# Performance work log

Hardware: AMD Instinct MI355X
Metric: run time of the kernel (lower is better)

Reference implementation:

```python
import jax, jax.numpy as jnp
import numpy as np


def setup_inputs() -> dict:
    key = jax.random.key(0)
    k1, k2 = jax.random.split(key)
    B, C, T, H, W = 4, 256, 8, 32, 32
    K = 1024  # num_embeddings
    z = jax.random.normal(k1, (B, C, T, H, W), dtype=jnp.float32)
    # original init: uniform(-1/K, 1/K)
    emb_weight = jax.random.uniform(k2, (K, C), dtype=jnp.float32,
                                    minval=-1.0 / K, maxval=1.0 / K)
    return {"z": z, "emb_weight": emb_weight}


def reference(z, emb_weight):
    B, C, T, H, W = z.shape
    # (B,C,T,H,W) -> (N, C) with N = B*T*H*W
    z_flat = jnp.transpose(z, (0, 2, 3, 4, 1)).reshape(-1, C)
    # squared L2 distances via ||a||^2 + ||b||^2 - 2 a.b  (fused, vectorized;
    # no python batching loop needed)
    d = (jnp.sum(z_flat * z_flat, axis=1, keepdims=True)
         + jnp.sum(emb_weight * emb_weight, axis=1)
         - 2.0 * z_flat @ emb_weight.T)  # (N, K)
    indices = jnp.argmin(d, axis=1)  # (N,)
    z_q = emb_weight[indices]  # (N, C) gather
    z_q = jnp.transpose(z_q.reshape(B, T, H, W, C), (0, 4, 1, 2, 3))
    # straight-through estimator
    z_q = z + jax.lax.stop_gradient(z_q - z)
    return z_q, indices.reshape(B, T, H, W)
```

## Files before the change

kernel.cpp:

```cpp
#include <hip/hip_runtime.h>
#include <hip/hip_bf16.h>


#define DEVI __device__ __forceinline__

typedef __attribute__((ext_vector_type(8))) short bf16x8;
typedef __attribute__((ext_vector_type(4))) float f32x4;

#define C_DIM   256
#define K_CODES 1024
#define S_DIM   8192
#define N_ROWS  32768
#define ZQ_ELEMS 8388608
#define TILE_M  64
#define NCHUNK  32
#define BAND1   1.0e-3f
#define REC_CAP 8192
#define UCAP    832
#define FLT_BIG 3.402823466e+38f

#define WS_EFR  0
#define WS_E2F  524288
#define WS_CNT  528384
#define WS_REC  528448

DEVI unsigned short f2b(float f) {
    unsigned u = __float_as_uint(f);
    u += 0x7FFFu + ((u >> 16) & 1u);
    return (unsigned short)(u >> 16);
}
DEVI unsigned umin2(unsigned a, unsigned b) { return a < b ? a : b; }
DEVI unsigned umax2(unsigned a, unsigned b) { return a > b ? a : b; }
DEVI unsigned long long ullmin2(unsigned long long a, unsigned long long b) {
    return a < b ? a : b;
}
DEVI float ntl(const float* p) { return __builtin_nontemporal_load(p); }
DEVI void nts(float* p, float v) { __builtin_nontemporal_store(v, p); }

DEVI f32x4 MF(bf16x8 a, bf16x8 b, f32x4 c) {
    return __builtin_amdgcn_mfma_f32_16x16x32_bf16(a, b, c, 0, 0, 0);
}
DEVI bf16x8 ldsfrag(const char* L, int row, int coff) {
    const int byte = row * 512 + (coff ^ ((row & 7) << 4));
    return *reinterpret_cast<const bf16x8*>(L + byte);
}

__global__ void vq_prep(const float* __restrict__ E,
                        unsigned short* __restrict__ efrag,
                        float* __restrict__ e2f, int* __restrict__ gcnt) {
    const int k = blockIdx.x;
    const int lane = threadIdx.x;
    if (k == 0 && lane == 0) *gcnt = 0;
    const float4 v = reinterpret_cast<const float4*>(E + (size_t)k * C_DIM)[lane];
    double s = (double)v.x * v.x + (double)v.y * v.y
             + (double)v.z * v.z + (double)v.w * v.w;
    ushort4 h;
    h.x = f2b(v.x); h.y = f2b(v.y); h.z = f2b(v.z); h.w = f2b(v.w);
    const int f = lane >> 1, half = lane & 1;
    const int ks = f >> 2, q = f & 3;
    const int jj = k & 15, wn = (k >> 4) & 1, chunk = k >> 5;
    char* dst = (char*)efrag + (size_t)chunk * 16384 + wn * 8192
              + ks * 1024 + (q * 16 + jj) * 16 + half * 8;
    *reinterpret_cast<ushort4*>(dst) = h;
#pragma unroll
    for (int m = 32; m; m >>= 1) s += __shfl_xor(s, m, 64);
    if (lane == 0) e2f[k] = (float)s;
}

__global__ __launch_bounds__(256, 2) void vq_main(
        const float* __restrict__ z, const float* __restrict__ E,
        const unsigned short* __restrict__ efrag,
        const float* __restrict__ e2f,
        float* __restrict__ out_zq, float* __restrict__ out_idx,
        int* __restrict__ gcnt, int2* __restrict__ grec) {
    __shared__ __align__(16) char smraw[65792];
    __shared__ float e2p[1024];
    __shared__ int   kfinA[64];
    __shared__ int   flagA[64];
    __shared__ float znS[64];
    __shared__ unsigned long long best64[64];
    __shared__ int   units[UCAP];
    __shared__ int   ucnt;

    const int tid = threadIdx.x;
    const int n0 = blockIdx.x * TILE_M;
    const int b  = n0 >> 13;
    const int s0 = n0 & (S_DIM - 1);

    {
        const float4 v = reinterpret_cast<const float4*>(e2f)[tid];
        float4 w; w.x = 1.0f + v.x; w.y = 1.0f + v.y;
        w.z = 1.0f + v.z; w.w = 1.0f + v.w;
        reinterpret_cast<float4*>(e2p)[tid] = w;
    }

    {
        const int s  = tid & 63;
        const int cg = tid >> 6;
        const float* zb = z + (size_t)b * (C_DIM * S_DIM) + s0 + s;
#pragma unroll
        for (int ci = 0; ci < 16; ++ci) {
            const int c = cg * 4 + ci * 16;
            ushort4 h;
            h.x = f2b(ntl(zb + (size_t)(c + 0) * S_DIM));
            h.y = f2b(ntl(zb + (size_t)(c + 1) * S_DIM));
            h.z = f2b(ntl(zb + (size_t)(c + 2) * S_DIM));
            h.w = f2b(ntl(zb + (size_t)(c + 3) * S_DIM));
            const int byte = s * 512 + ((c * 2) ^ ((s & 7) << 4));
            *reinterpret_cast<ushort4*>(smraw + byte) = h;
        }
    }
    __syncthreads();

    const int w    = tid >> 6;
    const int lane = tid & 63;
    const int wm   = w >> 1, wn = w & 1;
    const int q    = lane >> 4, jj = lane & 15;
    const int mycol = wn * 16 + jj;

    bf16x8 Ah0[8], Ah1[8];
    {
        const int r0 = wm * 32 + jj, r1 = r0 + 16;
#pragma unroll
        for (int ks = 0; ks < 8; ++ks) {
            const int coff = ks * 64 + q * 16;
            Ah0[ks] = ldsfrag(smraw, r0, coff);
            Ah1[ks] = ldsfrag(smraw, r1, coff);
        }
    }

    const char* gB = (const char*)efrag + (size_t)wn * 8192 + (size_t)lane * 16;

#define LOADB(BR, N)                                                          \
    { _Pragma("unroll")                                                       \
      for (int ks_ = 0; ks_ < 8; ++ks_)                                       \
          BR[ks_] = *reinterpret_cast<const bf16x8*>(                         \
              gB + (size_t)(N) * 16384 + ks_ * 1024); }

#define RCOMPUTE(BR, A0, A1)                                                  \
    { A0 = (f32x4){0.f, 0.f, 0.f, 0.f}; A1 = A0;                              \
      _Pragma("unroll")                                                       \
      for (int ks_ = 0; ks_ < 8; ++ks_) {                                     \
          A0 = MF(Ah0[ks_], BR[ks_], A0);                                     \
          A1 = MF(Ah1[ks_], BR[ks_], A1);                                     \
      } }

#define UPD(A0, A1, E2V, N)                                                   \
    { _Pragma("unroll")                                                       \
      for (int r = 0; r < 4; ++r) {                                           \
          unsigned t_ = (__float_as_uint(                                     \
              __builtin_fmaf(-2.f, A0[r], E2V)) & 0xFFFFFFE0u) | (unsigned)(N);\
          unsigned lo_ = umin2(K1[r], t_), hi_ = umax2(K1[r], t_);            \
          K1[r] = lo_; K2[r] = umin2(K2[r], hi_);                             \
          t_ = (__float_as_uint(                                              \
              __builtin_fmaf(-2.f, A1[r], E2V)) & 0xFFFFFFE0u) | (unsigned)(N);\
          lo_ = umin2(K1[4 + r], t_); hi_ = umax2(K1[4 + r], t_);             \
          K1[4 + r] = lo_; K2[4 + r] = umin2(K2[4 + r], hi_);                 \
      } }

    unsigned K1[8], K2[8];
#pragma unroll
    for (int i = 0; i < 8; ++i) { K1[i] = 0xFFFFFFFFu; K2[i] = 0xFFFFFFFFu; }

    bf16x8 Bc[8], Bn[8];
    LOADB(Bc, 0)
    LOADB(Bn, 1)
    f32x4 aA0, aA1, aB0, aB1;

#pragma unroll
    for (int p = 0; p < 16; ++p) {
        const int nA = 2 * p, nB = 2 * p + 1;
        RCOMPUTE(Bc, aA0, aA1)
        if (p < 15) LOADB(Bc, nA + 2)
        UPD(aA0, aA1, e2p[nA * 32 + mycol], nA)
        RCOMPUTE(Bn, aB0, aB1)
        if (p < 15) LOADB(Bn, nB + 2)
        UPD(aB0, aB1, e2p[nB * 32 + mycol], nB)
    }

    __syncthreads();
    if (tid == 0) ucnt = 0;
    for (int i = tid; i < UCAP; i += 256) units[i] = -1;
#pragma unroll
    for (int t = 0; t < 2; ++t) {
#pragma unroll
        for (int r = 0; r < 4; ++r) {
            const int sl = t * 4 + r;
            const int row = wm * 32 + t * 16 + q * 4 + r;
            *reinterpret_cast<int2*>(smraw + row * 272 + mycol * 8) =
                make_int2((int)K1[sl], (int)K2[sl]);
        }
    }
    __syncthreads();

    if (tid < 64) {
        const char* dmp = smraw + tid * 272;
        unsigned kmin = 0xFFFFFFFFu; int emin = 0;
#pragma unroll 4
        for (int e = 0; e < 32; ++e) {
            const unsigned k1 = (unsigned)
                reinterpret_cast<const int2*>(dmp + e * 8)->x;
            if (k1 < kmin) { kmin = k1; emin = e; }
        }
        const int kmincode = (int)((kmin & 31u) << 5) | emin;
        const float dminf = __uint_as_float(kmin & 0xFFFFFFE0u);
        const unsigned limk =
            (__float_as_uint(dminf + BAND1) & 0xFFFFFFE0u) | 31u;
        int cnt = 0, nfb = 0, fb0 = 0, fb1 = 0;
#pragma unroll 4
        for (int e = 0; e < 32; ++e) {
            const int2 v = *reinterpret_cast<const int2*>(dmp + e * 8);
            if ((unsigned)v.x <= limk) {
                const int code = (int)(((unsigned)v.x & 31u) << 5) | e;
                cnt += (code != kmincode);
            }
            if ((unsigned)v.y <= limk) {
                if (nfb == 0) fb0 = e; else if (nfb == 1) fb1 = e;
                ++nfb;
            }
        }
        kfinA[tid] = kmincode;
        flagA[tid] = 0;
        if (cnt > 0 || nfb > 0) {
            bool ov = (cnt > 16 || nfb > 2);
            if (!ov) {
                const int need = 1 + cnt + 32 * nfb;
                const int base = atomicAdd(&ucnt, need);
                if (base + need <= UCAP) {
                    flagA[tid] = 1;
                    best64[tid] = 0xFFFFFFFFFFFFFFFFull;
                    int p = base;
                    units[p++] = (tid << 10) | kmincode;
                    for (int e = 0; e < 32; ++e) {
                        const int2 v = *reinterpret_cast<const int2*>(dmp + e * 8);
                        if ((unsigned)v.x <= limk) {
                            const int code = (int)(((unsigned)v.x & 31u) << 5) | e;
                            if (code != kmincode) units[p++] = (tid << 10) | code;
                        }
                    }
                    if (nfb >= 1)
                        for (int c = 0; c < 32; ++c)
                            units[p++] = (tid << 10) | (c << 5) | fb0;
                    if (nfb >= 2)
                        for (int c = 0; c < 32; ++c)
                            units[p++] = (tid << 10) | (c << 5) | fb1;
                } else ov = true;
            }
            if (ov) {
                const int slot = atomicAdd(gcnt, 1);
                if (slot < REC_CAP) grec[slot] = make_int2(n0 + tid, kmincode);
            }
        }
    }
    __syncthreads();

    {
        const int s  = tid & 63;
        const int cg = tid >> 6;
        const float* zb = z + (size_t)b * (C_DIM * S_DIM) + s0 + s;
        float* zr = reinterpret_cast<float*>(smraw) + s * 257;
#pragma unroll
        for (int ci = 0; ci < 16; ++ci) {
            const int c = cg * 4 + ci * 16;
            zr[c + 0] = ntl(zb + (size_t)(c + 0) * S_DIM);
            zr[c + 1] = ntl(zb + (size_t)(c + 1) * S_DIM);
            zr[c + 2] = ntl(zb + (size_t)(c + 2) * S_DIM);
            zr[c + 3] = ntl(zb + (size_t)(c + 3) * S_DIM);
        }
    }
    __syncthreads();

    if (tid < 64 && flagA[tid]) {
        const float* zr = reinterpret_cast<const float*>(smraw) + tid * 257;
        double a0 = 0.0, a1 = 0.0, a2 = 0.0, a3 = 0.0;
#pragma unroll 8
        for (int c = 0; c < 256; c += 4) {
            const double v0 = zr[c], v1 = zr[c+1], v2 = zr[c+2], v3 = zr[c+3];
            a0 = fma(v0, v0, a0); a1 = fma(v1, v1, a1);
            a2 = fma(v2, v2, a2); a3 = fma(v3, v3, a3);
        }
        znS[tid] = (float)((a0 + a1) + (a2 + a3));
    }
    __syncthreads();

    {
        const int nu = (ucnt < UCAP) ? ucnt : UCAP;
        for (int u = tid; u < nu; u += 256) {
            const int enc = units[u];
            if (enc < 0) continue;
            const int row = enc >> 10, k = enc & 1023;
            const float* zr = reinterpret_cast<const float*>(smraw) + row * 257;
            const float* er = E + (size_t)k * C_DIM;
            double a0 = 0.0, a1 = 0.0, a2 = 0.0, a3 = 0.0;
#pragma unroll 8
            for (int c = 0; c < 256; c += 4) {
                a0 = fma((double)zr[c+0], (double)er[c+0], a0);
                a1 = fma((double)zr[c+1], (double)er[c+1], a1);
                a2 = fma((double)zr[c+2], (double)er[c+2], a2);
                a3 = fma((double)zr[c+3], (double)er[c+3], a3);
            }
            const float t32 = (float)((a0 + a1) + (a2 + a3));
            const float d = (znS[row] + e2f[k]) - 2.0f * t32;
            const unsigned long long key =
                ((unsigned long long)__float_as_uint(d) << 32) | (unsigned)k;
            atomicMin(&best64[row], key);
        }
    }
    __syncthreads();

    if (tid < 64) {
        if (flagA[tid])
            kfinA[tid] = (int)(best64[tid] & 0xFFFFFFFFull);
        nts(out_idx + n0 + tid, (float)kfinA[tid]);
    }

#pragma unroll
    for (int h = 0; h < 2; ++h) {
        __syncthreads();
        {
            const int slot = tid & 31;
            const int cg   = tid >> 5;
            const int kk   = kfinA[h * 32 + slot];
            const float4* er = reinterpret_cast<const float4*>(
                E + (size_t)kk * C_DIM + cg * 32);
            float* lb = reinterpret_cast<float*>(smraw) + slot * 257 + cg * 32;
#pragma unroll
            for (int i = 0; i < 8; ++i) {
                const float4 v = er[i];
                lb[4 * i + 0] = v.x; lb[4 * i + 1] = v.y;
                lb[4 * i + 2] = v.z; lb[4 * i + 3] = v.w;
            }
        }
        __syncthreads();
        {
            const int sg = tid & 31;
            const int cg = tid >> 5;
            float* ob = out_zq + (size_t)b * (C_DIM * S_DIM) + s0 + h * 32 + sg;
            const float* lr = reinterpret_cast<const float*>(smraw) + sg * 257;
#pragma unroll
            for (int i = 0; i < 32; ++i) {
                const int c = cg * 32 + i;
                nts(ob + (size_t)c * S_DIM, lr[c]);
            }
        }
    }
}

__global__ __launch_bounds__(256) void vq_fall(
        const float* __restrict__ z, const float* __restrict__ E,
        const float* __restrict__ e2f,
        const int* __restrict__ gcnt, const int2* __restrict__ grec,
        float* __restrict__ out_zq, float* __restrict__ out_idx) {
    __shared__ float zsh[256];
    __shared__ double dpart[4];
    __shared__ unsigned long long wbest[4];

    const int tid = threadIdx.x;
    const int w = tid >> 6, lane = tid & 63;
    int count = gcnt[0]; if (count > REC_CAP) count = REC_CAP;

    for (int ri = blockIdx.x; ri < count; ri += gridDim.x) {
        const int2 rc = grec[ri];
        const int n = rc.x, kmin = rc.y;
        const int b = n >> 13, s = n & (S_DIM - 1);
        __syncthreads();
        const float zc = z[((size_t)(b * C_DIM + tid)) * S_DIM + s];
        zsh[tid] = zc;
        double p = (double)zc * (double)zc;
#pragma unroll
        for (int m = 32; m; m >>= 1) p += __shfl_xor(p, m, 64);
        if (lane == 0) dpart[w] = p;
        __syncthreads();
        const float znf = (float)((dpart[0] + dpart[1]) + (dpart[2] + dpart[3]));

        unsigned long long best = 0xFFFFFFFFFFFFFFFFull;
        for (int j = 0; j < 4; ++j) {
            const int k = j * 256 + tid;
            const float4* er = reinterpret_cast<const float4*>(
                E + (size_t)k * C_DIM);
            double a0 = 0.0, a1 = 0.0, a2 = 0.0, a3 = 0.0;
#pragma unroll 8
            for (int i = 0; i < 64; ++i) {
                const float4 ev = er[i];
                const float4 zl = reinterpret_cast<const float4*>(zsh)[i];
                a0 = fma((double)zl.x, (double)ev.x, a0);
                a1 = fma((double)zl.y, (double)ev.y, a1);
                a2 = fma((double)zl.z, (double)ev.z, a2);
                a3 = fma((double)zl.w, (double)ev.w, a3);
            }
            const float t32 = (float)((a0 + a1) + (a2 + a3));
            const float d = (znf + e2f[k]) - 2.0f * t32;
            best = ullmin2(best,
                ((unsigned long long)__float_as_uint(d) << 32) | (unsigned)k);
        }
#pragma unroll
        for (int m = 32; m; m >>= 1)
            best = ullmin2(best, (unsigned long long)__shfl_xor(
                (long long)best, m, 64));
        if (lane == 0) wbest[w] = best;
        __syncthreads();
        const unsigned long long fin =
            ullmin2(ullmin2(wbest[0], wbest[1]), ullmin2(wbest[2], wbest[3]));
        const int bk = (int)(fin & 0xFFFFFFFFull);
        if (tid == 0) out_idx[n] = (float)bk;
        if (bk != kmin) {
            out_zq[((size_t)(b * C_DIM + tid)) * S_DIM + s] =
                E[(size_t)bk * C_DIM + tid];
        }
    }
}

extern "C" void kernel_launch(void* const* d_in, const int* in_sizes, int n_in,
                              void* d_out, int out_size, void* d_ws, size_t ws_size,
                              hipStream_t stream) {
    (void)in_sizes; (void)n_in; (void)out_size; (void)ws_size;
    const float* z = (const float*)d_in[0];
    const float* E = (const float*)d_in[1];
    char* wsb = (char*)d_ws;
    unsigned short* efrag = (unsigned short*)(wsb + WS_EFR);
    float* e2f = (float*)(wsb + WS_E2F);
    int*   cnt = (int*)  (wsb + WS_CNT);
    int2*  rec = (int2*) (wsb + WS_REC);
    float* out = (float*)d_out;

    vq_prep<<<dim3(K_CODES), dim3(64), 0, stream>>>(E, efrag, e2f, cnt);
    vq_main<<<dim3(N_ROWS / TILE_M), dim3(256), 0, stream>>>(
        z, E, efrag, e2f, out, out + ZQ_ELEMS, cnt, rec);
    vq_fall<<<dim3(1024), dim3(256), 0, stream>>>(
        z, E, e2f, cnt, rec, out, out + ZQ_ELEMS);
}
```

Measured before the change: 51.61 us.

## Stage codebook chunks into LDS via async global_load_lds double buffering

```diff
diff --git a/kernel.cpp b/kernel.cpp
--- a/kernel.cpp
+++ b/kernel.cpp
@@ -19,7 +19,7 @@
 #define UCAP    832
 #define FLT_BIG 3.402823466e+38f
 
-#define WS_EFR  0
+#define WS_EHI  0
 #define WS_E2F  524288
 #define WS_CNT  528384
 #define WS_REC  528448
@@ -44,9 +44,14 @@
     const int byte = row * 512 + (coff ^ ((row & 7) << 4));
     return *reinterpret_cast<const bf16x8*>(L + byte);
 }
+DEVI void gll16(const void* g, void* l) {
+    __builtin_amdgcn_global_load_lds(
+        (const __attribute__((address_space(1))) unsigned int*)g,
+        (__attribute__((address_space(3))) unsigned int*)l, 16, 0, 0);
+}
 
 __global__ void vq_prep(const float* __restrict__ E,
-                        unsigned short* __restrict__ efrag,
+                        unsigned short* __restrict__ ehi,
                         float* __restrict__ e2f, int* __restrict__ gcnt) {
     const int k = blockIdx.x;
     const int lane = threadIdx.x;
@@ -56,12 +61,8 @@
              + (double)v.z * v.z + (double)v.w * v.w;
     ushort4 h;
     h.x = f2b(v.x); h.y = f2b(v.y); h.z = f2b(v.z); h.w = f2b(v.w);
-    const int f = lane >> 1, half = lane & 1;
-    const int ks = f >> 2, q = f & 3;
-    const int jj = k & 15, wn = (k >> 4) & 1, chunk = k >> 5;
-    char* dst = (char*)efrag + (size_t)chunk * 16384 + wn * 8192
-              + ks * 1024 + (q * 16 + jj) * 16 + half * 8;
-    *reinterpret_cast<ushort4*>(dst) = h;
+    const int phys8 = ((((lane >> 1) ^ (k & 7)) << 1) | (lane & 1));
+    reinterpret_cast<ushort4*>(ehi + (size_t)k * C_DIM)[phys8] = h;
 #pragma unroll
     for (int m = 32; m; m >>= 1) s += __shfl_xor(s, m, 64);
     if (lane == 0) e2f[k] = (float)s;
@@ -69,7 +70,7 @@
 
 __global__ __launch_bounds__(256, 2) void vq_main(
         const float* __restrict__ z, const float* __restrict__ E,
-        const unsigned short* __restrict__ efrag,
+        const unsigned short* __restrict__ ehi,
         const float* __restrict__ e2f,
         float* __restrict__ out_zq, float* __restrict__ out_idx,
         int* __restrict__ gcnt, int2* __restrict__ grec) {
@@ -89,9 +90,9 @@
 
     {
         const float4 v = reinterpret_cast<const float4*>(e2f)[tid];
-        float4 w; w.x = 1.0f + v.x; w.y = 1.0f + v.y;
-        w.z = 1.0f + v.z; w.w = 1.0f + v.w;
-        reinterpret_cast<float4*>(e2p)[tid] = w;
+        float4 w2; w2.x = 1.0f + v.x; w2.y = 1.0f + v.y;
+        w2.z = 1.0f + v.z; w2.w = 1.0f + v.w;
+        reinterpret_cast<float4*>(e2p)[tid] = w2;
     }
 
     {
@@ -128,21 +129,32 @@
             Ah1[ks] = ldsfrag(smraw, r1, coff);
         }
     }
-
-    const char* gB = (const char*)efrag + (size_t)wn * 8192 + (size_t)lane * 16;
-
-#define LOADB(BR, N)                                                          \
+    __syncthreads();
+
+#define STAGE(N, BUF)                                                         \
     { _Pragma("unroll")                                                       \
-      for (int ks_ = 0; ks_ < 8; ++ks_)                                       \
-          BR[ks_] = *reinterpret_cast<const bf16x8*>(                         \
-              gB + (size_t)(N) * 16384 + ks_ * 1024); }
-
-#define RCOMPUTE(BR, A0, A1)                                                  \
-    { A0 = (f32x4){0.f, 0.f, 0.f, 0.f}; A1 = A0;                              \
+      for (int i_ = 0; i_ < 4; ++i_) {                                        \
+          const int j_ = w * 4 + i_;                                          \
+          gll16((const char*)ehi + ((size_t)(N) * 16 + j_) * 1024             \
+                    + (size_t)lane * 16,                                      \
+                smraw + (BUF) * 16384 + j_ * 1024);                           \
+      } }
+
+    STAGE(0, 0)
+    __syncthreads();
+    STAGE(1, 1)
+
+    const int browbyte = mycol * 512;
+    const int t0x = (q * 16) ^ ((jj & 7) << 4);
+
+#define COMPUTE(N, A0, A1)                                                    \
+    { const char* Lb = smraw + ((N) & 1) * 16384 + browbyte;                  \
+      A0 = (f32x4){0.f, 0.f, 0.f, 0.f}; A1 = A0;                              \
       _Pragma("unroll")                                                       \
-      for (int ks_ = 0; ks_ < 8; ++ks_) {                                     \
-          A0 = MF(Ah0[ks_], BR[ks_], A0);                                     \
-          A1 = MF(Ah1[ks_], BR[ks_], A1);                                     \
+      for (int ks = 0; ks < 8; ++ks) {                                        \
+          const bf16x8 bh = *reinterpret_cast<const bf16x8*>(                 \
+              Lb + ((ks * 64) ^ t0x));                                        \
+          A0 = MF(Ah0[ks], bh, A0); A1 = MF(Ah1[ks], bh, A1);                 \
       } }
 
 #define UPD(A0, A1, E2V, N)                                                   \
@@ -162,21 +174,26 @@
 #pragma unroll
     for (int i = 0; i < 8; ++i) { K1[i] = 0xFFFFFFFFu; K2[i] = 0xFFFFFFFFu; }
 
-    bf16x8 Bc[8], Bn[8];
-    LOADB(Bc, 0)
-    LOADB(Bn, 1)
     f32x4 aA0, aA1, aB0, aB1;
-
-#pragma unroll
-    for (int p = 0; p < 16; ++p) {
-        const int nA = 2 * p, nB = 2 * p + 1;
-        RCOMPUTE(Bc, aA0, aA1)
-        if (p < 15) LOADB(Bc, nA + 2)
-        UPD(aA0, aA1, e2p[nA * 32 + mycol], nA)
-        RCOMPUTE(Bn, aB0, aB1)
-        if (p < 15) LOADB(Bn, nB + 2)
-        UPD(aB0, aB1, e2p[nB * 32 + mycol], nB)
-    }
+    float e2A, e2B;
+    COMPUTE(0, aA0, aA1); e2A = e2p[mycol];
+
+    for (int p = 0; p < 15; ++p) {
+        const int n1 = 2 * p + 1;
+        __syncthreads();
+        STAGE(n1 + 1, 0)
+        COMPUTE(n1, aB0, aB1); e2B = e2p[n1 * 32 + mycol];
+        UPD(aA0, aA1, e2A, n1 - 1)
+        const int n2 = 2 * p + 2;
+        __syncthreads();
+        if (n2 + 1 < NCHUNK) STAGE(n2 + 1, 1)
+        COMPUTE(n2, aA0, aA1); e2A = e2p[n2 * 32 + mycol];
+        UPD(aB0, aB1, e2B, n2 - 1)
+    }
+    __syncthreads();
+    COMPUTE(31, aB0, aB1); e2B = e2p[31 * 32 + mycol];
+    UPD(aA0, aA1, e2A, 30)
+    UPD(aB0, aB1, e2B, 31)
 
     __syncthreads();
     if (tid == 0) ucnt = 0;
@@ -417,15 +434,15 @@
     const float* z = (const float*)d_in[0];
     const float* E = (const float*)d_in[1];
     char* wsb = (char*)d_ws;
-    unsigned short* efrag = (unsigned short*)(wsb + WS_EFR);
+    unsigned short* ehi = (unsigned short*)(wsb + WS_EHI);
     float* e2f = (float*)(wsb + WS_E2F);
     int*   cnt = (int*)  (wsb + WS_CNT);
     int2*  rec = (int2*) (wsb + WS_REC);
     float* out = (float*)d_out;
 
-    vq_prep<<<dim3(K_CODES), dim3(64), 0, stream>>>(E, efrag, e2f, cnt);
+    vq_prep<<<dim3(K_CODES), dim3(64), 0, stream>>>(E, ehi, e2f, cnt);
     vq_main<<<dim3(N_ROWS / TILE_M), dim3(256), 0, stream>>>(
-        z, E, efrag, e2f, out, out + ZQ_ELEMS, cnt, rec);
+        z, E, ehi, e2f, out, out + ZQ_ELEMS, cnt, rec);
     vq_fall<<<dim3(1024), dim3(256), 0, stream>>>(
         z, E, e2f, cnt, rec, out, out + ZQ_ELEMS);
 }
```

Result: slower. 58.93 us (+14.2%).
